# Performance work log

Hardware: AMD Instinct MI355X
Metric: run time of the kernel (lower is better)

Reference implementation:

```python
import jax, jax.numpy as jnp
import numpy as np

B, T, V, H = 128, 256, 512, 1024
EOS_ID = 1


def _onehot_seq(key, eos_pos):
    k1, = jax.random.split(key, 1)
    toks = jax.random.randint(k1, (B, T), 2, V)  # avoid 0/1 so EOS only where planted
    toks = toks.at[jnp.arange(B), eos_pos].set(EOS_ID)
    return jax.nn.one_hot(toks, V, dtype=jnp.float32)


def setup_inputs() -> dict:
    key = jax.random.key(0)
    ks = jax.random.split(key, 12)
    enc_eos = jax.random.randint(ks[0], (B,), T // 2, T)
    dec_eos = jax.random.randint(ks[1], (B,), T // 2, T)
    s = 0.05
    return {
        "encoder_inputs": _onehot_seq(ks[2], enc_eos),
        "decoder_inputs": _onehot_seq(ks[3], dec_eos),
        "enc_Wi": jax.random.normal(ks[4], (V, 4 * H), jnp.float32) * s,
        "enc_Wh": jax.random.normal(ks[5], (H, 4 * H), jnp.float32) * s,
        "enc_b": jnp.zeros((4 * H,), jnp.float32),
        "dec_Wi": jax.random.normal(ks[6], (V, 4 * H), jnp.float32) * s,
        "dec_Wh": jax.random.normal(ks[7], (H, 4 * H), jnp.float32) * s,
        "dec_b": jnp.zeros((4 * H,), jnp.float32),
        "dense_W": jax.random.normal(ks[8], (H, V), jnp.float32) * s,
        "dense_b": jnp.zeros((V,), jnp.float32),
    }


def get_sequence_lengths(seq, eos_id=EOS_ID):
    eos_row = seq[:, :, eos_id]                      # [B,T]
    eos_idx = jnp.argmax(eos_row == eos_id, axis=-1)  # first position hitting EOS
    found = eos_row[jnp.arange(seq.shape[0]), eos_idx] == eos_id
    return jnp.where(found, eos_idx + 1, seq.shape[1])


def lstm_scan(c0, h0, x_btv, Wi, Wh, b):
    """Scans an LSTM over time axis 1; returns (c_seq, h_seq) each [B,T,H]."""
    def step(carry, x):
        c, h = carry
        z = x @ Wi + h @ Wh + b                      # [B,4H]
        i, f, g, o = jnp.split(z, 4, axis=-1)
        c = jax.nn.sigmoid(f) * c + jax.nn.sigmoid(i) * jnp.tanh(g)
        h = jax.nn.sigmoid(o) * jnp.tanh(c)
        return (c, h), (c, h)
    xs = jnp.swapaxes(x_btv, 0, 1)                   # [T,B,V]
    _, (cs, hs) = jax.lax.scan(step, (c0, h0), xs)
    return jnp.swapaxes(cs, 0, 1), jnp.swapaxes(hs, 0, 1)


def reference(encoder_inputs, decoder_inputs, enc_Wi, enc_Wh, enc_b,
              dec_Wi, dec_Wh, dec_b, dense_W, dense_b):
    b = encoder_inputs.shape[0]
    # --- encoder ---
    lengths = get_sequence_lengths(encoder_inputs)
    idx = jnp.maximum(0, lengths - 1)
    c0 = jnp.zeros((b, H), encoder_inputs.dtype)
    h0 = jnp.zeros((b, H), encoder_inputs.dtype)
    cs, hs = lstm_scan(c0, h0, encoder_inputs, enc_Wi, enc_Wh, enc_b)
    ar = jnp.arange(b)
    c_enc, h_enc = cs[ar, idx], hs[ar, idx]          # carry at EOS step
    # --- decoder (teacher forcing on decoder_inputs[:, :-1]) ---
    _, hd = lstm_scan(c_enc, h_enc, decoder_inputs[:, :-1], dec_Wi, dec_Wh, dec_b)
    logits = hd @ dense_W + dense_b                  # [B,T-1,V]
    return logits
```

## Files before the change

### kernel.cpp

```cpp
#include <hip/hip_runtime.h>

#define Bv 128
#define Tv 256
#define Vv 512
#define Hv 1024
#define FH 4096
#define TD 255

typedef unsigned short ushort_t;
typedef __attribute__((ext_vector_type(8))) short bf16x8;
typedef __attribute__((ext_vector_type(4))) float f32x4;

__device__ __forceinline__ ushort_t f2bf(float f) {
    unsigned u = __float_as_uint(f);
    unsigned r = (u + 0x7fffu + ((u >> 16) & 1u)) >> 16;
    return (ushort_t)r;
}
__device__ __forceinline__ float bf2f(ushort_t h) {
    return __uint_as_float(((unsigned)h) << 16);
}
__device__ __forceinline__ float sigm(float x) {
    return 1.0f / (1.0f + expf(-x));
}

__global__ __launch_bounds__(256) void wsplit_t(
    const float* __restrict__ W, int K, int N,
    ushort_t* __restrict__ hiT, ushort_t* __restrict__ loT)
{
    __shared__ float ts[32][65];
    const int n0 = blockIdx.x * 64, k0 = blockIdx.y * 32;
    const int tid = threadIdx.x;
#pragma unroll
    for (int i = 0; i < 8; i++) {
        int f = tid + i * 256;
        int k = f >> 6, nn = f & 63;
        ts[k][nn] = W[(size_t)(k0 + k) * N + n0 + nn];
    }
    __syncthreads();
#pragma unroll
    for (int i = 0; i < 8; i++) {
        int f = tid + i * 256;
        int nn = f >> 5, k = f & 31;
        float v = ts[k][nn];
        ushort_t h = f2bf(v);
        ushort_t l = f2bf(v - bf2f(h));
        size_t o = (size_t)(n0 + nn) * K + k0 + k;
        hiT[o] = h;
        loT[o] = l;
    }
}

__global__ __launch_bounds__(256) void extract_tokens(
    const float* __restrict__ x, int* __restrict__ tok)
{
    int row = blockIdx.x * 4 + (threadIdx.x >> 6);
    int lane = threadIdx.x & 63;
    const float* p = x + (size_t)row * Vv;
    int found = -1;
#pragma unroll
    for (int i = 0; i < 8; i++)
        if (p[lane + i * 64] > 0.5f) found = lane + i * 64;
#pragma unroll
    for (int off = 32; off > 0; off >>= 1) {
        int o = __shfl_down(found, off);
        found = found > o ? found : o;
    }
    if (lane == 0) tok[row] = found;
}

__global__ void find_eos(const int* __restrict__ tok, int* __restrict__ idx)
{
    int b = threadIdx.x;
    int first = Tv - 1;
    for (int t = Tv - 1; t >= 0; t--)
        if (tok[b * Tv + t] == 1) first = t;
    idx[b] = first;
}

__global__ __launch_bounds__(256) void lstm_step(
    const ushort_t* __restrict__ WhiT, const ushort_t* __restrict__ WloT,
    const float* __restrict__ Wi,
    const float* __restrict__ bias,
    const int* __restrict__ tok, int t,
    const ushort_t* __restrict__ hin_hi, const ushort_t* __restrict__ hin_lo,
    ushort_t* __restrict__ hout_hi, ushort_t* __restrict__ hout_lo,
    float* __restrict__ c_state,
    ushort_t* __restrict__ hex_hi, ushort_t* __restrict__ hex_lo,
    const int* __restrict__ save_idx,
    float* __restrict__ c_save, ushort_t* __restrict__ hs_hi, ushort_t* __restrict__ hs_lo)
{
    __shared__ float z_s[32][68];
    const int tid = threadIdx.x;
    const int wave = tid >> 6, lane = tid & 63;
    const int wm = wave & 1, wn = wave >> 1;
    const int n = lane & 15, quad = lane >> 4;
    const int j0 = blockIdx.x * 16;
    const int b0 = blockIdx.y * 32;

    const size_t arow = (size_t)(b0 + wm * 16 + n) * Hv + quad * 8;
    const size_t g0 = (size_t)((2 * wn + 0) * Hv + j0 + n) * Hv + quad * 8;
    const size_t g1 = (size_t)((2 * wn + 1) * Hv + j0 + n) * Hv + quad * 8;

    f32x4 acc0 = {0.f, 0.f, 0.f, 0.f}, acc1 = {0.f, 0.f, 0.f, 0.f};

#pragma unroll 2
    for (int kc = 0; kc < Hv; kc += 32) {
        bf16x8 ahi = *(const bf16x8*)(hin_hi + arow + kc);
        bf16x8 alo = *(const bf16x8*)(hin_lo + arow + kc);
        bf16x8 b0h = *(const bf16x8*)(WhiT + g0 + kc);
        bf16x8 b0l = *(const bf16x8*)(WloT + g0 + kc);
        bf16x8 b1h = *(const bf16x8*)(WhiT + g1 + kc);
        bf16x8 b1l = *(const bf16x8*)(WloT + g1 + kc);
        acc0 = __builtin_amdgcn_mfma_f32_16x16x32_bf16(ahi, b0h, acc0, 0, 0, 0);
        acc1 = __builtin_amdgcn_mfma_f32_16x16x32_bf16(ahi, b1h, acc1, 0, 0, 0);
        acc0 = __builtin_amdgcn_mfma_f32_16x16x32_bf16(alo, b0h, acc0, 0, 0, 0);
        acc1 = __builtin_amdgcn_mfma_f32_16x16x32_bf16(alo, b1h, acc1, 0, 0, 0);
        acc0 = __builtin_amdgcn_mfma_f32_16x16x32_bf16(ahi, b0l, acc0, 0, 0, 0);
        acc1 = __builtin_amdgcn_mfma_f32_16x16x32_bf16(ahi, b1l, acc1, 0, 0, 0);
    }

    const int row0 = wm * 16 + quad * 4;
    const int cb0 = (2 * wn + 0) * 16 + n;
    const int cb1 = cb0 + 16;
#pragma unroll
    for (int r = 0; r < 4; r++) {
        z_s[row0 + r][cb0] = acc0[r];
        z_s[row0 + r][cb1] = acc1[r];
    }
    __syncthreads();

#pragma unroll
    for (int i = 0; i < 2; i++) {
        int p = tid + i * 256;
        int bl = p >> 4, jl = p & 15;
        int b = b0 + bl, col = j0 + jl;
        int tk = tok[b * Tv + t];
        const float* wr = Wi + (size_t)tk * FH + col;
        float zi = z_s[bl][jl]      + wr[0]        + bias[col];
        float zf = z_s[bl][16 + jl] + wr[Hv]       + bias[Hv + col];
        float zg = z_s[bl][32 + jl] + wr[2 * Hv]   + bias[2 * Hv + col];
        float zo = z_s[bl][48 + jl] + wr[3 * Hv]   + bias[3 * Hv + col];
        float si = sigm(zi), sf = sigm(zf), so = sigm(zo);
        float gg = tanhf(zg);
        size_t off = (size_t)b * Hv + col;
        float cn = sf * c_state[off] + si * gg;
        float hn = so * tanhf(cn);
        c_state[off] = cn;
        ushort_t hh = f2bf(hn);
        ushort_t hl = f2bf(hn - bf2f(hh));
        hout_hi[off] = hh;
        hout_lo[off] = hl;
        if (hex_hi) { hex_hi[off] = hh; hex_lo[off] = hl; }
        if (save_idx) {
            if (t == save_idx[b]) { c_save[off] = cn; hs_hi[off] = hh; hs_lo[off] = hl; }
        }
    }
}

__global__ __launch_bounds__(256) void dense_mfma(
    const ushort_t* __restrict__ Ahi, const ushort_t* __restrict__ Alo,
    const ushort_t* __restrict__ WhiT, const ushort_t* __restrict__ WloT,
    const float* __restrict__ bias, float* __restrict__ out)
{
    const int tid = threadIdx.x;
    const int wave = tid >> 6, lane = tid & 63;
    const int wm = wave & 1, wn = wave >> 1;
    const int n = lane & 15, quad = lane >> 4;
    const int m0 = blockIdx.y * 32 + wm * 16;
    const int c0 = blockIdx.x * 64 + wn * 32;

    const size_t arow = (size_t)(m0 + n) * Hv + quad * 8;
    const size_t g0 = (size_t)(c0 + 0 + n) * Hv + quad * 8;
    const size_t g1 = (size_t)(c0 + 16 + n) * Hv + quad * 8;

    f32x4 acc0 = {0.f, 0.f, 0.f, 0.f}, acc1 = {0.f, 0.f, 0.f, 0.f};

#pragma unroll 2
    for (int kc = 0; kc < Hv; kc += 32) {
        bf16x8 ahi = *(const bf16x8*)(Ahi + arow + kc);
        bf16x8 alo = *(const bf16x8*)(Alo + arow + kc);
        bf16x8 b0h = *(const bf16x8*)(WhiT + g0 + kc);
        bf16x8 b0l = *(const bf16x8*)(WloT + g0 + kc);
        bf16x8 b1h = *(const bf16x8*)(WhiT + g1 + kc);
        bf16x8 b1l = *(const bf16x8*)(WloT + g1 + kc);
        acc0 = __builtin_amdgcn_mfma_f32_16x16x32_bf16(ahi, b0h, acc0, 0, 0, 0);
        acc1 = __builtin_amdgcn_mfma_f32_16x16x32_bf16(ahi, b1h, acc1, 0, 0, 0);
        acc0 = __builtin_amdgcn_mfma_f32_16x16x32_bf16(alo, b0h, acc0, 0, 0, 0);
        acc1 = __builtin_amdgcn_mfma_f32_16x16x32_bf16(alo, b1h, acc1, 0, 0, 0);
        acc0 = __builtin_amdgcn_mfma_f32_16x16x32_bf16(ahi, b0l, acc0, 0, 0, 0);
        acc1 = __builtin_amdgcn_mfma_f32_16x16x32_bf16(ahi, b1l, acc1, 0, 0, 0);
    }

#pragma unroll
    for (int r = 0; r < 4; r++) {
        int row = m0 + quad * 4 + r;
        int tt = row >> 7, bb = row & 127;
        size_t o = ((size_t)bb * TD + tt) * Vv;
        int col0 = c0 + n, col1 = c0 + 16 + n;
        out[o + col0] = acc0[r] + bias[col0];
        out[o + col1] = acc1[r] + bias[col1];
    }
}

extern "C" void kernel_launch(void* const* d_in, const int* in_sizes, int n_in,
                              void* d_out, int out_size, void* d_ws, size_t ws_size,
                              hipStream_t stream)
{
    const float* enc_in  = (const float*)d_in[0];
    const float* dec_in  = (const float*)d_in[1];
    const float* enc_Wi  = (const float*)d_in[2];
    const float* enc_Wh  = (const float*)d_in[3];
    const float* enc_b   = (const float*)d_in[4];
    const float* dec_Wi  = (const float*)d_in[5];
    const float* dec_Wh  = (const float*)d_in[6];
    const float* dec_b   = (const float*)d_in[7];
    const float* dense_W = (const float*)d_in[8];
    const float* dense_b = (const float*)d_in[9];
    float* out = (float*)d_out;

    char* wp = (char*)d_ws;
    auto take = [&](size_t bytes) -> char* {
        char* p = wp;
        wp += (bytes + 255) & ~(size_t)255;
        return p;
    };

    ushort_t* hd_hi = (ushort_t*)take((size_t)TD * Bv * Hv * 2);
    ushort_t* hd_lo = (ushort_t*)take((size_t)TD * Bv * Hv * 2);
    ushort_t* eWhi  = (ushort_t*)take((size_t)FH * Hv * 2);
    ushort_t* eWlo  = (ushort_t*)take((size_t)FH * Hv * 2);
    ushort_t* dWhi  = (ushort_t*)take((size_t)FH * Hv * 2);
    ushort_t* dWlo  = (ushort_t*)take((size_t)FH * Hv * 2);
    ushort_t* nWhi  = (ushort_t*)take((size_t)Vv * Hv * 2);
    ushort_t* nWlo  = (ushort_t*)take((size_t)Vv * Hv * 2);
    ushort_t* hbh0  = (ushort_t*)take((size_t)Bv * Hv * 2);
    ushort_t* hbl0  = (ushort_t*)take((size_t)Bv * Hv * 2);
    ushort_t* hbh1  = (ushort_t*)take((size_t)Bv * Hv * 2);
    ushort_t* hbl1  = (ushort_t*)take((size_t)Bv * Hv * 2);
    ushort_t* hshi  = (ushort_t*)take((size_t)Bv * Hv * 2);
    ushort_t* hslo  = (ushort_t*)take((size_t)Bv * Hv * 2);
    float*    c_state = (float*)take((size_t)Bv * Hv * 4);
    float*    c_save  = (float*)take((size_t)Bv * Hv * 4);
    int*      etok  = (int*)take((size_t)Bv * Tv * 4);
    int*      dtok  = (int*)take((size_t)Bv * Tv * 4);
    int*      eidx  = (int*)take((size_t)Bv * 4);

    ushort_t* hbh[2] = {hbh0, hbh1};
    ushort_t* hbl[2] = {hbl0, hbl1};

    wsplit_t<<<dim3(FH / 64, Hv / 32), 256, 0, stream>>>(enc_Wh, Hv, FH, eWhi, eWlo);
    wsplit_t<<<dim3(FH / 64, Hv / 32), 256, 0, stream>>>(dec_Wh, Hv, FH, dWhi, dWlo);
    wsplit_t<<<dim3(Vv / 64, Hv / 32), 256, 0, stream>>>(dense_W, Hv, Vv, nWhi, nWlo);
    extract_tokens<<<Bv * Tv / 4, 256, 0, stream>>>(enc_in, etok);
    extract_tokens<<<Bv * Tv / 4, 256, 0, stream>>>(dec_in, dtok);
    find_eos<<<1, Bv, 0, stream>>>(etok, eidx);

    hipMemsetAsync(hbh0, 0, (size_t)Bv * Hv * 2, stream);
    hipMemsetAsync(hbl0, 0, (size_t)Bv * Hv * 2, stream);
    hipMemsetAsync(c_state, 0, (size_t)Bv * Hv * 4, stream);

    for (int t = 0; t < Tv; t++) {
        lstm_step<<<dim3(64, 4), 256, 0, stream>>>(
            eWhi, eWlo, enc_Wi, enc_b, etok, t,
            hbh[t & 1], hbl[t & 1], hbh[(t + 1) & 1], hbl[(t + 1) & 1],
            c_state, nullptr, nullptr, eidx, c_save, hshi, hslo);
    }

    hipMemcpyAsync(c_state, c_save, (size_t)Bv * Hv * 4, hipMemcpyDeviceToDevice, stream);
    hipMemcpyAsync(hbh0, hshi, (size_t)Bv * Hv * 2, hipMemcpyDeviceToDevice, stream);
    hipMemcpyAsync(hbl0, hslo, (size_t)Bv * Hv * 2, hipMemcpyDeviceToDevice, stream);

    for (int t = 0; t < TD; t++) {
        lstm_step<<<dim3(64, 4), 256, 0, stream>>>(
            dWhi, dWlo, dec_Wi, dec_b, dtok, t,
            hbh[t & 1], hbl[t & 1], hbh[(t + 1) & 1], hbl[(t + 1) & 1],
            c_state, hd_hi + (size_t)t * Bv * Hv, hd_lo + (size_t)t * Bv * Hv,
            nullptr, nullptr, nullptr, nullptr);
    }

    dense_mfma<<<dim3(Vv / 64, (TD * Bv) / 32), 256, 0, stream>>>(
        hd_hi, hd_lo, nWhi, nWlo, dense_b, out);
}
```

Measured before the change: 14.29 ms.

## Replace per-timestep LSTM launches with a persistent cooperative kernel using grid sync

Replaces the 511 per-timestep lstm_step launches with one cooperative persistent kernel of 256 blocks. Each block keeps its slice of the recurrent weights (hi/lo bf16 split) resident in LDS and splits K four ways, writing partial gate sums to global memory. Two grid-wide syncs per step separate the MFMA phase from the elementwise cell update, and the cell state is held in registers. This removes launch overhead and repeated weight reloads, at the cost of two grid barriers per step and a partial-sum round trip through global memory; if the cooperative launch fails, it falls back to the old per-step launches.

```diff
diff --git a/kernel.cpp b/kernel.cpp
--- a/kernel.cpp
+++ b/kernel.cpp
@@ -1,4 +1,5 @@
 #include <hip/hip_runtime.h>
+#include <hip/hip_cooperative_groups.h>
 
 #define Bv 128
 #define Tv 256
@@ -157,6 +158,154 @@
     }
 }
 
+struct PArgs {
+    const ushort_t *eWhiT, *eWloT, *dWhiT, *dWloT;
+    const float *eWi, *dWi, *eb, *db;
+    const int *etok, *dtok, *eidx;
+    const ushort_t *hz_hi, *hz_lo;
+    ushort_t *hb0_hi, *hb0_lo, *hb1_hi, *hb1_lo;
+    ushort_t *hsv_hi, *hsv_lo;
+    ushort_t *hd_hi, *hd_lo;
+    float* z_p;
+};
+
+__global__ __launch_bounds__(256) void lstm_persist(PArgs P)
+{
+    __shared__ ushort_t wlds[2][32][64][8];
+    cooperative_groups::grid_group grid = cooperative_groups::this_grid();
+
+    const int tid  = threadIdx.x;
+    const int wave = tid >> 6, lane = tid & 63;
+    const int n = lane & 15, quad = lane >> 4;
+    const int wm = wave & 1, wn = wave >> 1;
+    const int blk = blockIdx.x;
+    const int cgi = blk & 63, kg = blk >> 6;
+    const int j0 = cgi * 16;
+    const int k0 = kg * 256;
+
+    auto fill_w = [&](const ushort_t* hiT, const ushort_t* loT) {
+#pragma unroll
+        for (int i = 0; i < 16; i++) {
+            int id = tid + i * 256;
+            int half = id >> 11, rem = id & 2047;
+            int kch = rem & 31, c = rem >> 5;
+            const ushort_t* src = half ? loT : hiT;
+            bf16x8 v = *(const bf16x8*)(src +
+                (size_t)((c >> 4) * Hv + j0 + (c & 15)) * Hv + k0 + kch * 8);
+            *(bf16x8*)(&wlds[half][kch][c][0]) = v;
+        }
+    };
+
+    auto mfma_phase = [&](const ushort_t* hih, const ushort_t* hil) {
+        const f32x4 vzero = {0.f, 0.f, 0.f, 0.f};
+        f32x4 acc[4][2];
+#pragma unroll
+        for (int mi = 0; mi < 4; mi++) { acc[mi][0] = vzero; acc[mi][1] = vzero; }
+        const int cA = wn * 32 + n;
+        const size_t abase = (size_t)(wm * 64 + n) * Hv + k0 + quad * 8;
+#pragma unroll 2
+        for (int kc = 0; kc < 256; kc += 32) {
+            int kq = (kc >> 3) + quad;
+            bf16x8 b0h = *(const bf16x8*)(&wlds[0][kq][cA][0]);
+            bf16x8 b1h = *(const bf16x8*)(&wlds[0][kq][cA + 16][0]);
+            bf16x8 b0l = *(const bf16x8*)(&wlds[1][kq][cA][0]);
+            bf16x8 b1l = *(const bf16x8*)(&wlds[1][kq][cA + 16][0]);
+#pragma unroll
+            for (int mi = 0; mi < 4; mi++) {
+                bf16x8 ah = *(const bf16x8*)(hih + abase + (size_t)mi * 16 * Hv + kc);
+                bf16x8 al = *(const bf16x8*)(hil + abase + (size_t)mi * 16 * Hv + kc);
+                acc[mi][0] = __builtin_amdgcn_mfma_f32_16x16x32_bf16(ah, b0h, acc[mi][0], 0, 0, 0);
+                acc[mi][1] = __builtin_amdgcn_mfma_f32_16x16x32_bf16(ah, b1h, acc[mi][1], 0, 0, 0);
+                acc[mi][0] = __builtin_amdgcn_mfma_f32_16x16x32_bf16(al, b0h, acc[mi][0], 0, 0, 0);
+                acc[mi][1] = __builtin_amdgcn_mfma_f32_16x16x32_bf16(al, b1h, acc[mi][1], 0, 0, 0);
+                acc[mi][0] = __builtin_amdgcn_mfma_f32_16x16x32_bf16(ah, b0l, acc[mi][0], 0, 0, 0);
+                acc[mi][1] = __builtin_amdgcn_mfma_f32_16x16x32_bf16(ah, b1l, acc[mi][1], 0, 0, 0);
+            }
+        }
+#pragma unroll
+        for (int mi = 0; mi < 4; mi++)
+#pragma unroll
+            for (int gs = 0; gs < 2; gs++) {
+                int cloc = (2 * wn + gs) * 16 + n;
+#pragma unroll
+                for (int r = 0; r < 4; r++) {
+                    int b = wm * 64 + mi * 16 + quad * 4 + r;
+                    P.z_p[(((size_t)kg * 64 + cgi) * 128 + b) * 64 + cloc] = acc[mi][gs][r];
+                }
+            }
+    };
+
+    const int b_e0 = kg * 32 + (tid >> 4);
+    const int b_e1 = b_e0 + 16;
+    const int jp   = tid & 15;
+    const int j    = j0 + jp;
+
+    const float eb_0 = P.eb[j], eb_1 = P.eb[Hv + j], eb_2 = P.eb[2 * Hv + j], eb_3 = P.eb[3 * Hv + j];
+    const float db_0 = P.db[j], db_1 = P.db[Hv + j], db_2 = P.db[2 * Hv + j], db_3 = P.db[3 * Hv + j];
+    const int eidx0 = P.eidx[b_e0], eidx1 = P.eidx[b_e1];
+    float c0 = 0.f, c1 = 0.f, csv0 = 0.f, csv1 = 0.f;
+
+    auto do_elem = [&](int t, const int* tok, const float* Wi,
+                       float bz0, float bz1, float bz2, float bz3,
+                       int b, float& cc, ushort_t* oh, ushort_t* ol,
+                       int dec_t, int eidx_b, float& csv) {
+        int tk = tok[b * Tv + t];
+        float z0 = bz0, z1 = bz1, z2 = bz2, z3 = bz3;
+#pragma unroll
+        for (int q = 0; q < 4; q++) {
+            const float* zq = P.z_p + (((size_t)q * 64 + cgi) * 128 + b) * 64 + jp;
+            z0 += zq[0]; z1 += zq[16]; z2 += zq[32]; z3 += zq[48];
+        }
+        const float* wr = Wi + (size_t)tk * FH + j;
+        z0 += wr[0]; z1 += wr[Hv]; z2 += wr[2 * Hv]; z3 += wr[3 * Hv];
+        float si = sigm(z0), sf = sigm(z1), so = sigm(z3);
+        float gg = tanhf(z2);
+        float cn = sf * cc + si * gg; cc = cn;
+        float hn = so * tanhf(cn);
+        ushort_t hh = f2bf(hn);
+        ushort_t hl = f2bf(hn - bf2f(hh));
+        size_t off = (size_t)b * Hv + j;
+        oh[off] = hh; ol[off] = hl;
+        if (dec_t >= 0) {
+            P.hd_hi[(size_t)dec_t * (Bv * Hv) + off] = hh;
+            P.hd_lo[(size_t)dec_t * (Bv * Hv) + off] = hl;
+        } else if (t == eidx_b) {
+            csv = cn;
+            P.hsv_hi[off] = hh; P.hsv_lo[off] = hl;
+        }
+    };
+
+    fill_w(P.eWhiT, P.eWloT);
+    __syncthreads();
+    const ushort_t* ih = P.hz_hi;
+    const ushort_t* il = P.hz_lo;
+    for (int t = 0; t < Tv; t++) {
+        mfma_phase(ih, il);
+        grid.sync();
+        ushort_t* oh = (t & 1) ? P.hb1_hi : P.hb0_hi;
+        ushort_t* ol = (t & 1) ? P.hb1_lo : P.hb0_lo;
+        do_elem(t, P.etok, P.eWi, eb_0, eb_1, eb_2, eb_3, b_e0, c0, oh, ol, -1, eidx0, csv0);
+        do_elem(t, P.etok, P.eWi, eb_0, eb_1, eb_2, eb_3, b_e1, c1, oh, ol, -1, eidx1, csv1);
+        grid.sync();
+        ih = oh; il = ol;
+    }
+
+    fill_w(P.dWhiT, P.dWloT);
+    __syncthreads();
+    c0 = csv0; c1 = csv1;
+    ih = P.hsv_hi; il = P.hsv_lo;
+    for (int t = 0; t < TD; t++) {
+        mfma_phase(ih, il);
+        grid.sync();
+        ushort_t* oh = (t & 1) ? P.hb1_hi : P.hb0_hi;
+        ushort_t* ol = (t & 1) ? P.hb1_lo : P.hb0_lo;
+        do_elem(t, P.dtok, P.dWi, db_0, db_1, db_2, db_3, b_e0, c0, oh, ol, t, eidx0, csv0);
+        do_elem(t, P.dtok, P.dWi, db_0, db_1, db_2, db_3, b_e1, c1, oh, ol, t, eidx1, csv1);
+        grid.sync();
+        ih = oh; il = ol;
+    }
+}
+
 __global__ __launch_bounds__(256) void dense_mfma(
     const ushort_t* __restrict__ Ahi, const ushort_t* __restrict__ Alo,
     const ushort_t* __restrict__ WhiT, const ushort_t* __restrict__ WloT,
@@ -233,20 +382,20 @@
     ushort_t* dWlo  = (ushort_t*)take((size_t)FH * Hv * 2);
     ushort_t* nWhi  = (ushort_t*)take((size_t)Vv * Hv * 2);
     ushort_t* nWlo  = (ushort_t*)take((size_t)Vv * Hv * 2);
-    ushort_t* hbh0  = (ushort_t*)take((size_t)Bv * Hv * 2);
-    ushort_t* hbl0  = (ushort_t*)take((size_t)Bv * Hv * 2);
-    ushort_t* hbh1  = (ushort_t*)take((size_t)Bv * Hv * 2);
-    ushort_t* hbl1  = (ushort_t*)take((size_t)Bv * Hv * 2);
+    ushort_t* hzhi  = (ushort_t*)take((size_t)Bv * Hv * 2);
+    ushort_t* hzlo  = (ushort_t*)take((size_t)Bv * Hv * 2);
+    ushort_t* hb0h  = (ushort_t*)take((size_t)Bv * Hv * 2);
+    ushort_t* hb0l  = (ushort_t*)take((size_t)Bv * Hv * 2);
+    ushort_t* hb1h  = (ushort_t*)take((size_t)Bv * Hv * 2);
+    ushort_t* hb1l  = (ushort_t*)take((size_t)Bv * Hv * 2);
     ushort_t* hshi  = (ushort_t*)take((size_t)Bv * Hv * 2);
     ushort_t* hslo  = (ushort_t*)take((size_t)Bv * Hv * 2);
+    float*    z_p   = (float*)take((size_t)4 * Bv * FH * 4);
     float*    c_state = (float*)take((size_t)Bv * Hv * 4);
     float*    c_save  = (float*)take((size_t)Bv * Hv * 4);
     int*      etok  = (int*)take((size_t)Bv * Tv * 4);
     int*      dtok  = (int*)take((size_t)Bv * Tv * 4);
     int*      eidx  = (int*)take((size_t)Bv * 4);
-
-    ushort_t* hbh[2] = {hbh0, hbh1};
-    ushort_t* hbl[2] = {hbl0, hbl1};
 
     wsplit_t<<<dim3(FH / 64, Hv / 32), 256, 0, stream>>>(enc_Wh, Hv, FH, eWhi, eWlo);
     wsplit_t<<<dim3(FH / 64, Hv / 32), 256, 0, stream>>>(dec_Wh, Hv, FH, dWhi, dWlo);
@@ -255,27 +404,48 @@
     extract_tokens<<<Bv * Tv / 4, 256, 0, stream>>>(dec_in, dtok);
     find_eos<<<1, Bv, 0, stream>>>(etok, eidx);
 
-    hipMemsetAsync(hbh0, 0, (size_t)Bv * Hv * 2, stream);
-    hipMemsetAsync(hbl0, 0, (size_t)Bv * Hv * 2, stream);
-    hipMemsetAsync(c_state, 0, (size_t)Bv * Hv * 4, stream);
-
-    for (int t = 0; t < Tv; t++) {
-        lstm_step<<<dim3(64, 4), 256, 0, stream>>>(
-            eWhi, eWlo, enc_Wi, enc_b, etok, t,
-            hbh[t & 1], hbl[t & 1], hbh[(t + 1) & 1], hbl[(t + 1) & 1],
-            c_state, nullptr, nullptr, eidx, c_save, hshi, hslo);
-    }
-
-    hipMemcpyAsync(c_state, c_save, (size_t)Bv * Hv * 4, hipMemcpyDeviceToDevice, stream);
-    hipMemcpyAsync(hbh0, hshi, (size_t)Bv * Hv * 2, hipMemcpyDeviceToDevice, stream);
-    hipMemcpyAsync(hbl0, hslo, (size_t)Bv * Hv * 2, hipMemcpyDeviceToDevice, stream);
-
-    for (int t = 0; t < TD; t++) {
-        lstm_step<<<dim3(64, 4), 256, 0, stream>>>(
-            dWhi, dWlo, dec_Wi, dec_b, dtok, t,
-            hbh[t & 1], hbl[t & 1], hbh[(t + 1) & 1], hbl[(t + 1) & 1],
-            c_state, hd_hi + (size_t)t * Bv * Hv, hd_lo + (size_t)t * Bv * Hv,
-            nullptr, nullptr, nullptr, nullptr);
+    hipMemsetAsync(hzhi, 0, (size_t)Bv * Hv * 2, stream);
+    hipMemsetAsync(hzlo, 0, (size_t)Bv * Hv * 2, stream);
+
+    PArgs pa;
+    pa.eWhiT = eWhi; pa.eWloT = eWlo; pa.dWhiT = dWhi; pa.dWloT = dWlo;
+    pa.eWi = enc_Wi; pa.dWi = dec_Wi; pa.eb = enc_b; pa.db = dec_b;
+    pa.etok = etok; pa.dtok = dtok; pa.eidx = eidx;
+    pa.hz_hi = hzhi; pa.hz_lo = hzlo;
+    pa.hb0_hi = hb0h; pa.hb0_lo = hb0l; pa.hb1_hi = hb1h; pa.hb1_lo = hb1l;
+    pa.hsv_hi = hshi; pa.hsv_lo = hslo;
+    pa.hd_hi = hd_hi; pa.hd_lo = hd_lo;
+    pa.z_p = z_p;
+
+    void* kargs[] = { (void*)&pa };
+    hipError_t ce = hipLaunchCooperativeKernel((void*)lstm_persist,
+                                               dim3(256), dim3(256), kargs, 0u, stream);
+    if (ce != hipSuccess) {
+        (void)hipGetLastError();
+
+        hipMemsetAsync(hzhi, 0, (size_t)Bv * Hv * 2, stream);
+        hipMemsetAsync(hzlo, 0, (size_t)Bv * Hv * 2, stream);
+        hipMemsetAsync(c_state, 0, (size_t)Bv * Hv * 4, stream);
+
+        ushort_t* hbh[2] = {hzhi, hb0h};
+        ushort_t* hbl[2] = {hzlo, hb0l};
+
+        for (int t = 0; t < Tv; t++) {
+            lstm_step<<<dim3(64, 4), 256, 0, stream>>>(
+                eWhi, eWlo, enc_Wi, enc_b, etok, t,
+                hbh[t & 1], hbl[t & 1], hbh[(t + 1) & 1], hbl[(t + 1) & 1],
+                c_state, nullptr, nullptr, eidx, c_save, hshi, hslo);
+        }
+        hipMemcpyAsync(c_state, c_save, (size_t)Bv * Hv * 4, hipMemcpyDeviceToDevice, stream);
+        hipMemcpyAsync(hbh[0], hshi, (size_t)Bv * Hv * 2, hipMemcpyDeviceToDevice, stream);
+        hipMemcpyAsync(hbl[0], hslo, (size_t)Bv * Hv * 2, hipMemcpyDeviceToDevice, stream);
+        for (int t = 0; t < TD; t++) {
+            lstm_step<<<dim3(64, 4), 256, 0, stream>>>(
+                dWhi, dWlo, dec_Wi, dec_b, dtok, t,
+                hbh[t & 1], hbl[t & 1], hbh[(t + 1) & 1], hbl[(t + 1) & 1],
+                c_state, hd_hi + (size_t)t * Bv * Hv, hd_lo + (size_t)t * Bv * Hv,
+                nullptr, nullptr, nullptr, nullptr);
+        }
     }
 
     dense_mfma<<<dim3(Vv / 64, (TD * Bv) / 32), 256, 0, stream>>>(
```

After: 39.04 ms. 2.73x slower.

## Split LSTM step K-reduction across four wave groups with 1024-thread blocks

Applied to the files above, without the earlier changes.

Each lstm_step block now uses 1024 threads, with four wave groups each covering a quarter of the hidden K dimension. Partial gate sums go into a larger shared buffer and are added in the epilogue. Token, Wi row, bias, c_state and save-index loads are issued before the MFMA loop so their latency overlaps the matmul. The aim is to shorten the serial K loop per step for this latency-bound recurrence, at the cost of more shared memory, more register pressure, and half the threads sitting idle during the epilogue.

```diff
diff --git a/kernel.cpp b/kernel.cpp
--- a/kernel.cpp
+++ b/kernel.cpp
@@ -77,7 +77,7 @@
     idx[b] = first;
 }
 
-__global__ __launch_bounds__(256) void lstm_step(
+__global__ __launch_bounds__(1024, 4) void lstm_step(
     const ushort_t* __restrict__ WhiT, const ushort_t* __restrict__ WloT,
     const float* __restrict__ Wi,
     const float* __restrict__ bias,
@@ -89,22 +89,43 @@
     const int* __restrict__ save_idx,
     float* __restrict__ c_save, ushort_t* __restrict__ hs_hi, ushort_t* __restrict__ hs_lo)
 {
-    __shared__ float z_s[32][68];
+    __shared__ float z_s[4][32][68];
     const int tid = threadIdx.x;
     const int wave = tid >> 6, lane = tid & 63;
-    const int wm = wave & 1, wn = wave >> 1;
+    const int wk = wave >> 2;
+    const int wm = wave & 1, wn = (wave >> 1) & 1;
     const int n = lane & 15, quad = lane >> 4;
     const int j0 = blockIdx.x * 16;
     const int b0 = blockIdx.y * 32;
-
-    const size_t arow = (size_t)(b0 + wm * 16 + n) * Hv + quad * 8;
-    const size_t g0 = (size_t)((2 * wn + 0) * Hv + j0 + n) * Hv + quad * 8;
-    const size_t g1 = (size_t)((2 * wn + 1) * Hv + j0 + n) * Hv + quad * 8;
+    const int k0 = wk * 256;
+
+    const bool act = tid < 512;
+    const int bl = tid >> 4, jl = tid & 15;
+    const int b_e = b0 + bl, col = j0 + jl;
+    float w0 = 0.f, w1 = 0.f, w2 = 0.f, w3 = 0.f;
+    float bz0 = 0.f, bz1 = 0.f, bz2 = 0.f, bz3 = 0.f;
+    float c_old = 0.f;
+    int sidx = -1;
+    size_t off = 0;
+    if (act) {
+        int tk = tok[b_e * Tv + t];
+        const float* wr = Wi + (size_t)tk * FH + col;
+        w0 = wr[0]; w1 = wr[Hv]; w2 = wr[2 * Hv]; w3 = wr[3 * Hv];
+        bz0 = bias[col];          bz1 = bias[Hv + col];
+        bz2 = bias[2 * Hv + col]; bz3 = bias[3 * Hv + col];
+        off = (size_t)b_e * Hv + col;
+        c_old = c_state[off];
+        if (save_idx) sidx = save_idx[b_e];
+    }
+
+    const size_t arow = (size_t)(b0 + wm * 16 + n) * Hv + k0 + quad * 8;
+    const size_t g0 = (size_t)((2 * wn + 0) * Hv + j0 + n) * Hv + k0 + quad * 8;
+    const size_t g1 = (size_t)((2 * wn + 1) * Hv + j0 + n) * Hv + k0 + quad * 8;
 
     f32x4 acc0 = {0.f, 0.f, 0.f, 0.f}, acc1 = {0.f, 0.f, 0.f, 0.f};
 
 #pragma unroll 2
-    for (int kc = 0; kc < Hv; kc += 32) {
+    for (int kc = 0; kc < 256; kc += 32) {
         bf16x8 ahi = *(const bf16x8*)(hin_hi + arow + kc);
         bf16x8 alo = *(const bf16x8*)(hin_lo + arow + kc);
         bf16x8 b0h = *(const bf16x8*)(WhiT + g0 + kc);
@@ -124,26 +145,23 @@
     const int cb1 = cb0 + 16;
 #pragma unroll
     for (int r = 0; r < 4; r++) {
-        z_s[row0 + r][cb0] = acc0[r];
-        z_s[row0 + r][cb1] = acc1[r];
+        z_s[wk][row0 + r][cb0] = acc0[r];
+        z_s[wk][row0 + r][cb1] = acc1[r];
     }
     __syncthreads();
 
-#pragma unroll
-    for (int i = 0; i < 2; i++) {
-        int p = tid + i * 256;
-        int bl = p >> 4, jl = p & 15;
-        int b = b0 + bl, col = j0 + jl;
-        int tk = tok[b * Tv + t];
-        const float* wr = Wi + (size_t)tk * FH + col;
-        float zi = z_s[bl][jl]      + wr[0]        + bias[col];
-        float zf = z_s[bl][16 + jl] + wr[Hv]       + bias[Hv + col];
-        float zg = z_s[bl][32 + jl] + wr[2 * Hv]   + bias[2 * Hv + col];
-        float zo = z_s[bl][48 + jl] + wr[3 * Hv]   + bias[3 * Hv + col];
-        float si = sigm(zi), sf = sigm(zf), so = sigm(zo);
-        float gg = tanhf(zg);
-        size_t off = (size_t)b * Hv + col;
-        float cn = sf * c_state[off] + si * gg;
+    if (act) {
+        float z0 = bz0 + w0, z1 = bz1 + w1, z2 = bz2 + w2, z3 = bz3 + w3;
+#pragma unroll
+        for (int q = 0; q < 4; q++) {
+            z0 += z_s[q][bl][jl];
+            z1 += z_s[q][bl][16 + jl];
+            z2 += z_s[q][bl][32 + jl];
+            z3 += z_s[q][bl][48 + jl];
+        }
+        float si = sigm(z0), sf = sigm(z1), so = sigm(z3);
+        float gg = tanhf(z2);
+        float cn = sf * c_old + si * gg;
         float hn = so * tanhf(cn);
         c_state[off] = cn;
         ushort_t hh = f2bf(hn);
@@ -152,7 +170,7 @@
         hout_lo[off] = hl;
         if (hex_hi) { hex_hi[off] = hh; hex_lo[off] = hl; }
         if (save_idx) {
-            if (t == save_idx[b]) { c_save[off] = cn; hs_hi[off] = hh; hs_lo[off] = hl; }
+            if (t == sidx) { c_save[off] = cn; hs_hi[off] = hh; hs_lo[off] = hl; }
         }
     }
 }
@@ -260,7 +278,7 @@
     hipMemsetAsync(c_state, 0, (size_t)Bv * Hv * 4, stream);
 
     for (int t = 0; t < Tv; t++) {
-        lstm_step<<<dim3(64, 4), 256, 0, stream>>>(
+        lstm_step<<<dim3(64, 4), 1024, 0, stream>>>(
             eWhi, eWlo, enc_Wi, enc_b, etok, t,
             hbh[t & 1], hbl[t & 1], hbh[(t + 1) & 1], hbl[(t + 1) & 1],
             c_state, nullptr, nullptr, eidx, c_save, hshi, hslo);
@@ -271,7 +289,7 @@
     hipMemcpyAsync(hbl0, hslo, (size_t)Bv * Hv * 2, hipMemcpyDeviceToDevice, stream);
 
     for (int t = 0; t < TD; t++) {
-        lstm_step<<<dim3(64, 4), 256, 0, stream>>>(
+        lstm_step<<<dim3(64, 4), 1024, 0, stream>>>(
             dWhi, dWlo, dec_Wi, dec_b, dtok, t,
             hbh[t & 1], hbl[t & 1], hbh[(t + 1) & 1], hbl[(t + 1) & 1],
             c_state, hd_hi + (size_t)t * Bv * Hv, hd_lo + (size_t)t * Bv * Hv,
```

Result: faster. 13.53 ms (-5.4%).
